# Kernel tuning notes

Measured on AMD Instinct MI355X. Metric: run time of the kernel, lower is better.

Reference implementation:

```python
import jax, jax.numpy as jnp
import numpy as np

EMBED_DIM = 2048
NUM_HEADS = 16
BLOCK_SIZE = 128


def setup_inputs() -> dict:
    key = jax.random.key(0)
    k1, k2, k3 = jax.random.split(key, 3)
    B, S, E = 2, 4096, EMBED_DIM
    x = jax.random.normal(k1, (B, S, E), dtype=jnp.float32)
    # small init so attention logits are in a sane range
    w_qkv = jax.random.normal(k2, (3 * E, E), dtype=jnp.float32) * 0.02
    w_out = jax.random.normal(k3, (E, E), dtype=jnp.float32) * 0.02
    b_out = jnp.zeros((E,), dtype=jnp.float32)
    return {"x": x, "w_qkv": w_qkv, "w_out": w_out, "b_out": b_out}


def _flash_attention_v2(q, k, v, block_size, scale):
    # q,k,v: [B,H,S,D]; S divisible by block_size.
    # Faithful to the torch module, including its extra l_ij factor in the
    # output rescaling (out += beta*l_ij/l_new * (p @ v)).
    B, H, S, D = q.shape
    nb = S // block_size
    qb = q.reshape(B, H, nb, block_size, D)          # all query blocks at once
    kb = k.reshape(B, H, nb, block_size, D).transpose(2, 0, 1, 3, 4)  # [nb,B,H,bs,D]
    vb = v.reshape(B, H, nb, block_size, D).transpose(2, 0, 1, 3, 4)

    out0 = jnp.zeros_like(qb)
    l0 = jnp.zeros((B, H, nb, block_size, 1), dtype=q.dtype)
    m0 = jnp.full((B, H, nb, block_size, 1), -jnp.inf, dtype=q.dtype)

    def step(carry, kv):
        out, l, m = carry
        k_j, v_j = kv  # [B,H,bs,D]
        s = jnp.einsum('bhnqd,bhkd->bhnqk', qb, k_j) * scale  # [B,H,nb,bs,bs]
        m_ij = jnp.max(s, axis=-1, keepdims=True)
        p = jnp.exp(s - m_ij)
        l_ij = jnp.sum(p, axis=-1, keepdims=True)
        m_new = jnp.maximum(m, m_ij)
        alpha = jnp.exp(m - m_new)
        beta = jnp.exp(m_ij - m_new)
        l_new = alpha * l + beta * l_ij
        pv = jnp.einsum('bhnqk,bhkd->bhnqd', p, v_j)
        out_new = (alpha * l / l_new) * out + (beta * l_ij / l_new) * pv
        return (out_new, l_new, m_new), None

    (out, _, _), _ = jax.lax.scan(step, (out0, l0, m0), (kb, vb))
    return out.reshape(B, H, S, D)


def reference(x, w_qkv, w_out, b_out):
    B, S, E = x.shape
    H = NUM_HEADS
    D = E // H
    scale = 1.0 / np.sqrt(D).astype(np.float32)
    qkv = (x @ w_qkv.T).reshape(B, S, 3, H, D)
    q, k, v = jnp.moveaxis(qkv, 2, 0)            # each [B,S,H,D]
    q = q.transpose(0, 2, 1, 3)                   # [B,H,S,D]
    k = k.transpose(0, 2, 1, 3)
    v = v.transpose(0, 2, 1, 3)
    out = _flash_attention_v2(q, k, v, BLOCK_SIZE, scale)  # [B,H,S,D]
    out = out.transpose(0, 2, 1, 3).reshape(B, S, E)
    return out @ w_out.T + b_out
```

## Files before the change

### kernel.cpp

```cpp
#include <hip/hip_runtime.h>
#include <hip/hip_bf16.h>
#include <stdint.h>

#define DEV __device__ __forceinline__

typedef __attribute__((ext_vector_type(8))) short short8;
typedef __attribute__((ext_vector_type(4))) float f32x4;

#define B_ 2
#define S_ 4096
#define E_ 2048
#define H_ 16
#define D_ 128

#define BAR() asm volatile("s_barrier" ::: "memory")
#define LGKM0() asm volatile("s_waitcnt lgkmcnt(0)" ::: "memory")
#define VMC(N) asm volatile("s_waitcnt vmcnt(" #N ")" ::: "memory")

DEV unsigned short f2bf(float x) {
  union { float f; uint32_t u; } a; a.f = x;
  uint32_t r = a.u + 0x7fffu + ((a.u >> 16) & 1u);
  return (unsigned short)(r >> 16);
}

DEV unsigned int cvt_pk_bf16(float a, float b) {
  unsigned int r;
  asm("v_cvt_pk_bf16_f32 %0, %1, %2" : "=v"(r) : "v"(a), "v"(b));
  return r;
}

DEV float exp2f_(float x) { return __builtin_amdgcn_exp2f(x); }

DEV void glds16(const void* g, void* l) {
  __builtin_amdgcn_global_load_lds(
      (const __attribute__((address_space(1))) uint32_t*)g,
      (__attribute__((address_space(3))) uint32_t*)l, 16, 0, 0);
}

__global__ __launch_bounds__(256) void cvtk3(
    const float* __restrict__ x, const float* __restrict__ wq,
    const float* __restrict__ wo, unsigned short* __restrict__ xb,
    unsigned short* __restrict__ wqb, unsigned short* __restrict__ wob) {
  const int n1 = (B_ * S_ * E_) / 4, n2 = (3 * E_ * E_) / 4, n3 = (E_ * E_) / 4;
  int bid = blockIdx.x;
  const float4* s;
  ushort4* d;
  int n, b0, nb;
  if (bid < 1024)      { s = (const float4*)x;  d = (ushort4*)xb;  n = n1; b0 = 0;    nb = 1024; }
  else if (bid < 1792) { s = (const float4*)wq; d = (ushort4*)wqb; n = n2; b0 = 1024; nb = 768; }
  else                 { s = (const float4*)wo; d = (ushort4*)wob; n = n3; b0 = 1792; nb = 256; }
  for (int i = (bid - b0) * 256 + threadIdx.x; i < n; i += nb * 256) {
    float4 v = s[i];
    ushort4 o;
    o.x = f2bf(v.x); o.y = f2bf(v.y); o.z = f2bf(v.z); o.w = f2bf(v.w);
    d[i] = o;
  }
}

template<int OUT_F32, int VSPLIT>
__global__ __launch_bounds__(512, 2) void gemm256(
    const unsigned short* __restrict__ A,
    const unsigned short* __restrict__ Bm,
    void* __restrict__ Cp,
    const float* __restrict__ bias,
    unsigned short* __restrict__ vt,
    int M, int N, int K, int nbn)
{
  __shared__ __align__(16) unsigned char lds[131072];
  const int NT = K >> 6;
  const int K2 = K * 2;
  int cpx = gridDim.x >> 3;
  int bid = (blockIdx.x & 7) * cpx + (blockIdx.x >> 3);
  int bm = bid / nbn, bn = bid % nbn;
  int m0 = bm * 256, n0 = bn * 256;
  int t = threadIdx.x, lane = t & 63, wv = t >> 6;
  int lo = lane & 15, hi = lane >> 4;
  int wm = wv >> 2, wn = wv & 3;

  int colsw = ((t & 7) * 16) ^ (((t >> 3) & 7) << 4);
  const unsigned char* gA = (const unsigned char*)A + (size_t)(m0 + (t >> 3)) * K2 + colsw;
  const unsigned char* gB = (const unsigned char*)Bm + (size_t)(n0 + (t >> 3)) * K2 + colsw;

  int swzl = (lo & 7) << 4;
  int colk0 = (hi * 16) ^ swzl;
  int colk1 = (64 + hi * 16) ^ swzl;
  unsigned char* rdA = lds + wm * 16384 + lo * 128;
  unsigned char* rdB = lds + 32768 + (wn >> 1) * 16384 + ((wn & 1) * 64 + lo) * 128;

  f32x4 acc[8][4] = {};

  auto STG = [&](int isA, int d, int h, int kt) {
    if (kt >= NT) return;
    const unsigned char* g = (isA ? gA : gB) + (size_t)h * 128 * K2 + (size_t)kt * 128;
    unsigned char* l = lds + (isA ? 0 : 32768) + d * 65536 + h * 16384 + wv * 1024;
    glds16(g, l);
    glds16(g + (size_t)64 * K2, l + 8192);
  };
  auto DSA = [&](int d, int g4, int colk, short8* dst) {
#pragma unroll
    for (int i = 0; i < 4; ++i)
      dst[i] = *(const short8*)(rdA + d * 65536 + (g4 * 4 + i) * 2048 + colk);
  };
  auto DSB = [&](int d, int colk, short8* dst) {
#pragma unroll
    for (int i = 0; i < 4; ++i)
      dst[i] = *(const short8*)(rdB + d * 65536 + i * 2048 + colk);
  };
  auto MM = [&](int g4, short8* a, short8* b) {
    __builtin_amdgcn_s_setprio(1);
#pragma unroll
    for (int i = 0; i < 4; ++i)
#pragma unroll
      for (int j = 0; j < 4; ++j)
        acc[g4 * 4 + i][j] =
            __builtin_amdgcn_mfma_f32_16x16x32_bf16(a[i], b[j], acc[g4 * 4 + i][j], 0, 0, 0);
    __builtin_amdgcn_s_setprio(0);
  };

  STG(1, 0, 0, 0); STG(1, 0, 1, 0); STG(0, 0, 0, 0); STG(0, 0, 1, 0);
  STG(0, 1, 0, 1); STG(0, 1, 1, 1);
  VMC(4);
  BAR();

  short8 aT[4], aU[4], b0v[4], b1v[4];
  const int TL = (NT >> 1) - 1;
  for (int it = 0; it <= TL; ++it) {
    int j0 = 2 * it;
    DSA(0, 0, colk0, aT); DSB(0, colk0, b0v);
    STG(1, 1, 0, j0 + 1);
    BAR(); MM(0, aT, b0v); LGKM0(); BAR();
    DSA(0, 1, colk0, aU); DSB(0, colk1, b1v);
    STG(1, 1, 1, j0 + 1);
    BAR(); MM(1, aU, b0v); LGKM0(); BAR();
    DSA(0, 0, colk1, aT);
    STG(0, 0, 0, j0 + 2);
    BAR(); MM(0, aT, b1v); LGKM0(); BAR();
    DSA(0, 1, colk1, aU);
    STG(0, 0, 1, j0 + 2);
    BAR(); MM(1, aU, b1v); LGKM0();
    if (it == TL) { VMC(0); } else { VMC(4); }
    BAR();
    DSA(1, 0, colk0, aT); DSB(1, colk0, b0v);
    STG(1, 0, 0, j0 + 2);
    BAR(); MM(0, aT, b0v); LGKM0(); BAR();
    DSA(1, 1, colk0, aU); DSB(1, colk1, b1v);
    STG(1, 0, 1, j0 + 2);
    BAR(); MM(1, aU, b0v); LGKM0(); BAR();
    DSA(1, 0, colk1, aT);
    STG(0, 1, 0, j0 + 3);
    BAR(); MM(0, aT, b1v); LGKM0(); BAR();
    DSA(1, 1, colk1, aU);
    STG(0, 1, 1, j0 + 3);
    BAR(); MM(1, aU, b1v); LGKM0(); VMC(4);
    BAR();
  }

  if constexpr (VSPLIT) {
    if (bn >= 16) {
#pragma unroll
      for (int mf = 0; mf < 8; ++mf)
#pragma unroll
        for (int nf = 0; nf < 4; ++nf) {
          int row0 = wm * 128 + mf * 16 + hi * 4;
          int col = wn * 64 + nf * 16 + lo;
          uint2 pk;
          pk.x = (unsigned int)f2bf(acc[mf][nf][0]) | ((unsigned int)f2bf(acc[mf][nf][1]) << 16);
          pk.y = (unsigned int)f2bf(acc[mf][nf][2]) | ((unsigned int)f2bf(acc[mf][nf][3]) << 16);
          *(uint2*)(lds + col * 512 + ((row0 * 2) ^ ((col & 7) << 4))) = pk;
        }
      __syncthreads();
      int col = t & 255;
      int half = t >> 8;
      int nv = n0 + col - 4096;
      int hh = nv >> 7, dd = nv & 127;
      int b = m0 >> 12, s0 = m0 & 4095;
      unsigned short* vrow = vt + (((size_t)b * H_ + hh) * D_ + dd) * S_ + s0;
#pragma unroll
      for (int jj = 0; jj < 16; ++jj) {
        int j = half * 16 + jj;
        uint4 v = *(const uint4*)(lds + col * 512 + 16 * (j ^ (col & 7)));
        *(uint4*)(vrow + j * 8) = v;
      }
      return;
    }
  }

  if constexpr (OUT_F32) {
    float* C = (float*)Cp;
#pragma unroll
    for (int mf = 0; mf < 8; ++mf)
#pragma unroll
      for (int nf = 0; nf < 4; ++nf) {
        int row = m0 + wm * 128 + mf * 16 + hi * 4;
        int col = n0 + wn * 64 + nf * 16 + lo;
        float bv = bias[col];
#pragma unroll
        for (int r = 0; r < 4; ++r)
          C[(size_t)(row + r) * N + col] = acc[mf][nf][r] + bv;
      }
  } else {
    unsigned short* C = (unsigned short*)Cp;
#pragma unroll
    for (int mf = 0; mf < 8; ++mf)
#pragma unroll
      for (int nf = 0; nf < 4; ++nf) {
        int row = m0 + wm * 128 + mf * 16 + hi * 4;
        int col = n0 + wn * 64 + nf * 16 + lo;
#pragma unroll
        for (int r = 0; r < 4; ++r)
          C[(size_t)(row + r) * N + col] = f2bf(acc[mf][nf][r]);
      }
  }
}

__global__ __launch_bounds__(512, 2) void attn_fwd(
    const unsigned short* __restrict__ qkv,
    const unsigned short* __restrict__ vt,
    unsigned short* __restrict__ abuf)
{
  __shared__ __align__(16) unsigned char lds[65536];
  unsigned char* lK = lds;
  unsigned char* lV = lds + 32768;

  int bid = (blockIdx.x & 7) * 64 + (blockIdx.x >> 3);
  int qb = bid & 15, bh = bid >> 4;
  int h = bh & 15, b = bh >> 4;
  int t = threadIdx.x, lane = t & 63, wv = t >> 6;
  int hi = lane >> 4, lo = lane & 15;
  int q0 = qb * 256;
  const float c1 = 0.12751744f;

  short8 qf[2][4];
#pragma unroll
  for (int qj = 0; qj < 2; ++qj) {
    const unsigned short* qbase =
        qkv + ((((size_t)b * S_ + q0 + wv * 32 + qj * 16 + lo) * 3 + 0) * H_ + h) * D_;
#pragma unroll
    for (int ks = 0; ks < 4; ++ks)
      qf[qj][ks] = *(const short8*)(qbase + ks * 32 + hi * 8);
  }

  int sw = ((t & 15) * 16) ^ (((t >> 4) & 7) << 4);
  const unsigned char* gkb =
      (const unsigned char*)(qkv + (((size_t)b * S_ * 3 + 1) * H_ + h) * D_) +
      (size_t)(t >> 4) * 12288 + sw;
  const unsigned char* gvb =
      (const unsigned char*)(vt + ((size_t)b * H_ + h) * D_ * S_) +
      (size_t)(t >> 4) * 8192 + sw;
  unsigned char* lkd = lK + wv * 1024;
  unsigned char* lvd = lV + wv * 1024;

  f32x4 oacc[8][2] = {};
  float m_run[2] = {-__builtin_inff(), -__builtin_inff()};
  float l_run[2] = {0.f, 0.f};
  union PW { unsigned int u[4]; short8 s; };
  PW pp[2][4];

#pragma unroll
  for (int i = 0; i < 4; ++i) {
    glds16(gkb + i * 393216, lkd + i * 8192);
    glds16(gvb + i * 262144, lvd + i * 8192);
  }

  for (int jb = 0; jb < 32; ++jb) {
    VMC(0);
    BAR();

    f32x4 sacc[8][2];
    __builtin_amdgcn_s_setprio(1);
#pragma unroll
    for (int kf = 0; kf < 8; ++kf) {
      int kvr = kf * 16 + lo;
      int swz = (kvr & 7) << 4;
      sacc[kf][0] = f32x4{0.f, 0.f, 0.f, 0.f};
      sacc[kf][1] = f32x4{0.f, 0.f, 0.f, 0.f};
#pragma unroll
      for (int ks = 0; ks < 4; ++ks) {
        short8 kfr = *(const short8*)(lK + kvr * 256 + ((ks * 64 + hi * 16) ^ swz));
        sacc[kf][0] = __builtin_amdgcn_mfma_f32_16x16x32_bf16(kfr, qf[0][ks], sacc[kf][0], 0, 0, 0);
        sacc[kf][1] = __builtin_amdgcn_mfma_f32_16x16x32_bf16(kfr, qf[1][ks], sacc[kf][1], 0, 0, 0);
      }
    }
    __builtin_amdgcn_s_setprio(0);

    float m2[2], li[2], coef[2];
#pragma unroll
    for (int qj = 0; qj < 2; ++qj) {
      float mk[8];
#pragma unroll
      for (int kf = 0; kf < 8; ++kf)
        mk[kf] = fmaxf(fmaxf(sacc[kf][qj][0], sacc[kf][qj][1]),
                       fmaxf(sacc[kf][qj][2], sacc[kf][qj][3]));
      float ma = fmaxf(fmaxf(mk[0], mk[1]), fmaxf(mk[2], mk[3]));
      float mb = fmaxf(fmaxf(mk[4], mk[5]), fmaxf(mk[6], mk[7]));
      float mloc = fmaxf(ma, mb);
      mloc = fmaxf(mloc, __shfl_xor(mloc, 16));
      mloc = fmaxf(mloc, __shfl_xor(mloc, 32));
      m2[qj] = mloc * c1;
      float sk[8];
#pragma unroll
      for (int kf = 0; kf < 8; ++kf) {
        float p0 = exp2f_(fmaf(sacc[kf][qj][0], c1, -m2[qj]));
        float p1 = exp2f_(fmaf(sacc[kf][qj][1], c1, -m2[qj]));
        float p2 = exp2f_(fmaf(sacc[kf][qj][2], c1, -m2[qj]));
        float p3 = exp2f_(fmaf(sacc[kf][qj][3], c1, -m2[qj]));
        sacc[kf][qj][0] = p0; sacc[kf][qj][1] = p1;
        sacc[kf][qj][2] = p2; sacc[kf][qj][3] = p3;
        sk[kf] = (p0 + p1) + (p2 + p3);
      }
      float sa = (sk[0] + sk[1]) + (sk[2] + sk[3]);
      float sb = (sk[4] + sk[5]) + (sk[6] + sk[7]);
      float lloc = sa + sb;
      lloc += __shfl_xor(lloc, 16);
      lloc += __shfl_xor(lloc, 32);
      li[qj] = lloc;
    }

    if (__all(m2[0] <= m_run[0] && m2[1] <= m_run[1])) {
#pragma unroll
      for (int qj = 0; qj < 2; ++qj) {
        coef[qj] = exp2f_(m2[qj] - m_run[qj]) * li[qj];
        l_run[qj] += coef[qj];
      }
    } else {
      float alpha[2];
#pragma unroll
      for (int qj = 0; qj < 2; ++qj) {
        float mn = fmaxf(m_run[qj], m2[qj]);
        alpha[qj] = exp2f_(m_run[qj] - mn);
        coef[qj] = exp2f_(m2[qj] - mn) * li[qj];
        l_run[qj] = alpha[qj] * l_run[qj] + coef[qj];
        m_run[qj] = mn;
      }
#pragma unroll
      for (int df = 0; df < 8; ++df)
#pragma unroll
        for (int qj = 0; qj < 2; ++qj)
#pragma unroll
          for (int r = 0; r < 4; ++r) oacc[df][qj][r] *= alpha[qj];
    }

#pragma unroll
    for (int qj = 0; qj < 2; ++qj) {
      float cf = coef[qj];
#pragma unroll
      for (int ks = 0; ks < 4; ++ks) {
        unsigned int a0 = cvt_pk_bf16(sacc[2 * ks][qj][0] * cf, sacc[2 * ks][qj][1] * cf);
        unsigned int b0 = cvt_pk_bf16(sacc[2 * ks + 1][qj][0] * cf, sacc[2 * ks + 1][qj][1] * cf);
        unsigned int a1 = cvt_pk_bf16(sacc[2 * ks][qj][2] * cf, sacc[2 * ks][qj][3] * cf);
        unsigned int b1 = cvt_pk_bf16(sacc[2 * ks + 1][qj][2] * cf, sacc[2 * ks + 1][qj][3] * cf);
        asm("v_permlane32_swap_b32 %0, %1" : "+v"(a0), "+v"(b0));
        asm("v_permlane16_swap_b32 %0, %1" : "+v"(a0), "+v"(b0));
        asm("v_permlane32_swap_b32 %0, %1" : "+v"(a1), "+v"(b1));
        asm("v_permlane16_swap_b32 %0, %1" : "+v"(a1), "+v"(b1));
        pp[qj][ks].u[0] = a0;
        pp[qj][ks].u[1] = a1;
        pp[qj][ks].u[2] = b0;
        pp[qj][ks].u[3] = b1;
      }
    }

    __builtin_amdgcn_s_setprio(1);
#pragma unroll
    for (int ks = 0; ks < 4; ++ks) {
#pragma unroll
      for (int df = 0; df < 8; ++df) {
        int dr = df * 16 + lo;
        short8 vf = *(const short8*)(lV + dr * 256 + ((ks * 64 + hi * 16) ^ ((dr & 7) << 4)));
        oacc[df][0] = __builtin_amdgcn_mfma_f32_16x16x32_bf16(vf, pp[0][ks].s, oacc[df][0], 0, 0, 0);
        oacc[df][1] = __builtin_amdgcn_mfma_f32_16x16x32_bf16(vf, pp[1][ks].s, oacc[df][1], 0, 0, 0);
      }
    }
    __builtin_amdgcn_s_setprio(0);

    BAR();
    if (jb < 31) {
      size_t kvK = (size_t)(jb + 1) * 1572864;
      size_t kvV = (size_t)(jb + 1) * 256;
#pragma unroll
      for (int i = 0; i < 4; ++i) {
        glds16(gkb + kvK + i * 393216, lkd + i * 8192);
        glds16(gvb + kvV + i * 262144, lvd + i * 8192);
      }
    }
  }

  BAR();
#pragma unroll
  for (int qj = 0; qj < 2; ++qj) {
    int rq = wv * 32 + qj * 16 + lo;
    int swzq = (rq & 7) << 4;
    float inv = 1.0f / l_run[qj];
#pragma unroll
    for (int df = 0; df < 8; ++df) {
      uint2 pk;
      pk.x = cvt_pk_bf16(oacc[df][qj][0] * inv, oacc[df][qj][1] * inv);
      pk.y = cvt_pk_bf16(oacc[df][qj][2] * inv, oacc[df][qj][3] * inv);
      *(uint2*)(lds + rq * 256 + ((df * 32 + hi * 8) ^ swzq)) = pk;
    }
  }
  __syncthreads();
#pragma unroll
  for (int i = 0; i < 8; ++i) {
    int row = i * 32 + (t >> 4);
    int c = t & 15;
    uint4 val = *(const uint4*)(lds + row * 256 + ((c * 16) ^ ((row & 7) << 4)));
    unsigned short* dst = abuf + (((size_t)b * S_ + q0 + row) * H_ + h) * D_ + c * 8;
    *(uint4*)dst = val;
  }
}

extern "C" void kernel_launch(void* const* d_in, const int* in_sizes, int n_in,
                              void* d_out, int out_size, void* d_ws, size_t ws_size,
                              hipStream_t stream) {
  const float* x = (const float*)d_in[0];
  const float* w_qkv = (const float*)d_in[1];
  const float* w_out = (const float*)d_in[2];
  const float* b_out = (const float*)d_in[3];
  float* out = (float*)d_out;
  char* ws = (char*)d_ws;

  unsigned short* xb    = (unsigned short*)(ws);
  unsigned short* wqkvb = (unsigned short*)(ws + 33554432);
  unsigned short* woutb = (unsigned short*)(ws + 58720256);
  unsigned short* qkvb  = (unsigned short*)(ws + 67108864);
  unsigned short* vtb   = (unsigned short*)(ws + 167772160);
  unsigned short* abuf  = xb;

  cvtk3<<<2048, 256, 0, stream>>>(x, w_qkv, w_out, xb, wqkvb, woutb);

  gemm256<0, 1><<<768, 512, 0, stream>>>(xb, wqkvb, (void*)qkvb, nullptr, vtb,
                                         B_ * S_, 3 * E_, E_, 24);
  attn_fwd<<<512, 512, 0, stream>>>(qkvb, vtb, abuf);
  gemm256<1, 0><<<256, 512, 0, stream>>>(abuf, woutb, (void*)out, b_out, nullptr,
                                         B_ * S_, E_, E_, 8);
}
```

Measured before the change: 625.2 us.

## Software-pipeline QK and PV across KV blocks with P staged through LDS

```diff
diff --git a/kernel.cpp b/kernel.cpp
--- a/kernel.cpp
+++ b/kernel.cpp
@@ -218,9 +218,9 @@
     const unsigned short* __restrict__ vt,
     unsigned short* __restrict__ abuf)
 {
-  __shared__ __align__(16) unsigned char lds[65536];
+  __shared__ __align__(16) unsigned char lds[163840];
   unsigned char* lK = lds;
-  unsigned char* lV = lds + 32768;
+  unsigned char* lP = lds + 98304;
 
   int bid = (blockIdx.x & 7) * 64 + (blockIdx.x >> 3);
   int qb = bid & 15, bh = bid >> 4;
@@ -248,25 +248,25 @@
       (const unsigned char*)(vt + ((size_t)b * H_ + h) * D_ * S_) +
       (size_t)(t >> 4) * 8192 + sw;
   unsigned char* lkd = lK + wv * 1024;
-  unsigned char* lvd = lV + wv * 1024;
 
   f32x4 oacc[8][2] = {};
   float m_run[2] = {-__builtin_inff(), -__builtin_inff()};
   float l_run[2] = {0.f, 0.f};
-  union PW { unsigned int u[4]; short8 s; };
-  PW pp[2][4];
-
-#pragma unroll
-  for (int i = 0; i < 4; ++i) {
-    glds16(gkb + i * 393216, lkd + i * 8192);
-    glds16(gvb + i * 262144, lvd + i * 8192);
-  }
-
-  for (int jb = 0; jb < 32; ++jb) {
-    VMC(0);
-    BAR();
-
-    f32x4 sacc[8][2];
+  f32x4 sacc[8][2];
+  float coef[2];
+
+  auto STAGE = [&](int n) {
+    size_t kvK = (size_t)n * 1572864;
+    size_t kvV = (size_t)n * 256;
+    unsigned char* lvd = lds + 32768 + ((n & 1) << 15) + wv * 1024;
+#pragma unroll
+    for (int i = 0; i < 4; ++i) {
+      glds16(gkb + kvK + (size_t)i * 393216, lkd + i * 8192);
+      glds16(gvb + kvV + (size_t)i * 262144, lvd + i * 8192);
+    }
+  };
+
+  auto QK = [&]() {
     __builtin_amdgcn_s_setprio(1);
 #pragma unroll
     for (int kf = 0; kf < 8; ++kf) {
@@ -282,8 +282,27 @@
       }
     }
     __builtin_amdgcn_s_setprio(0);
-
-    float m2[2], li[2], coef[2];
+  };
+
+  auto PV = [&](const unsigned char* vb) {
+    int rq0 = wv * 32 + lo, rq1 = rq0 + 16;
+    int sz0 = (rq0 & 7) << 4;
+#pragma unroll
+    for (int ks = 0; ks < 4; ++ks) {
+      short8 pf0 = *(const short8*)(lP + rq0 * 256 + ((ks * 64 + hi * 16) ^ sz0));
+      short8 pf1 = *(const short8*)(lP + rq1 * 256 + ((ks * 64 + hi * 16) ^ sz0));
+#pragma unroll
+      for (int df = 0; df < 8; ++df) {
+        int dr = df * 16 + lo;
+        short8 vf = *(const short8*)(vb + dr * 256 + ((ks * 64 + hi * 16) ^ ((dr & 7) << 4)));
+        oacc[df][0] = __builtin_amdgcn_mfma_f32_16x16x32_bf16(vf, pf0, oacc[df][0], 0, 0, 0);
+        oacc[df][1] = __builtin_amdgcn_mfma_f32_16x16x32_bf16(vf, pf1, oacc[df][1], 0, 0, 0);
+      }
+    }
+  };
+
+  auto SOFTMAX = [&]() {
+    float m2[2], li[2];
 #pragma unroll
     for (int qj = 0; qj < 2; ++qj) {
       float mk[8];
@@ -315,7 +334,6 @@
       lloc += __shfl_xor(lloc, 32);
       li[qj] = lloc;
     }
-
     if (__all(m2[0] <= m_run[0] && m2[1] <= m_run[1])) {
 #pragma unroll
       for (int qj = 0; qj < 2; ++qj) {
@@ -339,51 +357,44 @@
 #pragma unroll
           for (int r = 0; r < 4; ++r) oacc[df][qj][r] *= alpha[qj];
     }
-
+  };
+
+  auto PACK = [&]() {
 #pragma unroll
     for (int qj = 0; qj < 2; ++qj) {
+      int rq = wv * 32 + qj * 16 + lo;
+      int swzq = (rq & 7) << 4;
       float cf = coef[qj];
 #pragma unroll
-      for (int ks = 0; ks < 4; ++ks) {
-        unsigned int a0 = cvt_pk_bf16(sacc[2 * ks][qj][0] * cf, sacc[2 * ks][qj][1] * cf);
-        unsigned int b0 = cvt_pk_bf16(sacc[2 * ks + 1][qj][0] * cf, sacc[2 * ks + 1][qj][1] * cf);
-        unsigned int a1 = cvt_pk_bf16(sacc[2 * ks][qj][2] * cf, sacc[2 * ks][qj][3] * cf);
-        unsigned int b1 = cvt_pk_bf16(sacc[2 * ks + 1][qj][2] * cf, sacc[2 * ks + 1][qj][3] * cf);
-        asm("v_permlane32_swap_b32 %0, %1" : "+v"(a0), "+v"(b0));
-        asm("v_permlane16_swap_b32 %0, %1" : "+v"(a0), "+v"(b0));
-        asm("v_permlane32_swap_b32 %0, %1" : "+v"(a1), "+v"(b1));
-        asm("v_permlane16_swap_b32 %0, %1" : "+v"(a1), "+v"(b1));
-        pp[qj][ks].u[0] = a0;
-        pp[qj][ks].u[1] = a1;
-        pp[qj][ks].u[2] = b0;
-        pp[qj][ks].u[3] = b1;
-      }
-    }
-
-    __builtin_amdgcn_s_setprio(1);
-#pragma unroll
-    for (int ks = 0; ks < 4; ++ks) {
-#pragma unroll
-      for (int df = 0; df < 8; ++df) {
-        int dr = df * 16 + lo;
-        short8 vf = *(const short8*)(lV + dr * 256 + ((ks * 64 + hi * 16) ^ ((dr & 7) << 4)));
-        oacc[df][0] = __builtin_amdgcn_mfma_f32_16x16x32_bf16(vf, pp[0][ks].s, oacc[df][0], 0, 0, 0);
-        oacc[df][1] = __builtin_amdgcn_mfma_f32_16x16x32_bf16(vf, pp[1][ks].s, oacc[df][1], 0, 0, 0);
-      }
-    }
-    __builtin_amdgcn_s_setprio(0);
-
+      for (int kf = 0; kf < 8; ++kf) {
+        uint2 pk;
+        pk.x = cvt_pk_bf16(sacc[kf][qj][0] * cf, sacc[kf][qj][1] * cf);
+        pk.y = cvt_pk_bf16(sacc[kf][qj][2] * cf, sacc[kf][qj][3] * cf);
+        *(uint2*)(lP + rq * 256 + ((kf * 32 + hi * 8) ^ swzq)) = pk;
+      }
+    }
+  };
+
+  STAGE(0);
+  VMC(0);
+  BAR();
+  QK();
+  SOFTMAX();
+  BAR();
+  STAGE(1);
+  PACK();
+
+  for (int jb = 1; jb < 32; ++jb) {
+    VMC(0);
     BAR();
-    if (jb < 31) {
-      size_t kvK = (size_t)(jb + 1) * 1572864;
-      size_t kvV = (size_t)(jb + 1) * 256;
-#pragma unroll
-      for (int i = 0; i < 4; ++i) {
-        glds16(gkb + kvK + i * 393216, lkd + i * 8192);
-        glds16(gvb + kvV + i * 262144, lvd + i * 8192);
-      }
-    }
-  }
+    QK();
+    PV(lds + 32768 + (((jb - 1) & 1) << 15));
+    SOFTMAX();
+    BAR();
+    if (jb < 31) STAGE(jb + 1);
+    PACK();
+  }
+  PV(lds + 65536);
 
   BAR();
 #pragma unroll
```

Result: slower. 984.5 us (+57.5%).
